# Kernel optimization log

Measured on AMD Instinct MI355X. Metric: run time of the kernel, lower is better.

Reference implementation:

```python
import jax, jax.numpy as jnp
import numpy as np

HEADS = 8
DIM_HEAD = 64
SCALE = DIM_HEAD ** -0.5


def setup_inputs() -> dict:
    key = jax.random.key(0)
    ks = jax.random.split(key, 6)
    b, n, d_model = 16, 1024, 512
    inner = HEADS * DIM_HEAD  # 512
    std = d_model ** -0.5
    return {
        "x": jax.random.normal(ks[0], (b, n, d_model), jnp.float32),
        "Wq": jax.random.normal(ks[1], (inner, d_model), jnp.float32) * std,
        "Wk": jax.random.normal(ks[2], (inner, d_model), jnp.float32) * std,
        "Wv": jax.random.normal(ks[3], (inner, d_model), jnp.float32) * std,
        "rel_bias": jax.random.normal(ks[4], (HEADS, n, n), jnp.float32) * 0.02,
        "Wo": jax.random.normal(ks[5], (d_model, inner), jnp.float32) * std,
        "bo": jnp.zeros((d_model,), jnp.float32),
    }


def reference(x, Wq, Wk, Wv, rel_bias, Wo, bo):
    b, n, _ = x.shape
    # projections (Linear with weight of shape [out, in], no bias)
    def proj_heads(W):
        t = jnp.einsum('bnc,ec->bne', x, W)             # [b, n, inner]
        return t.reshape(b, n, HEADS, DIM_HEAD).transpose(0, 2, 1, 3)  # [b, h, n, d]
    q = proj_heads(Wq)
    k = proj_heads(Wk)
    v = proj_heads(Wv)
    sim = jnp.einsum('bhid,bhjd->bhij', q, k) * SCALE
    sim = sim + rel_bias[None]                          # additive rel-pos bias
    attn = jax.nn.softmax(sim, axis=-1)
    out = jnp.einsum('bhij,bhjd->bhid', attn, v)        # [b, h, n, d]
    out = out.transpose(0, 2, 1, 3).reshape(b, n, HEADS * DIM_HEAD)
    return jnp.einsum('bne,ce->bnc', out, Wo) + bo
```

## Files before the change

kernel.cpp:

```cpp
#include <hip/hip_runtime.h>

typedef unsigned short u16;
typedef short short8 __attribute__((ext_vector_type(8)));
typedef float fx4 __attribute__((ext_vector_type(4)));
typedef u16 u16x4 __attribute__((ext_vector_type(4)));
typedef u16 u16x8 __attribute__((ext_vector_type(8)));


__device__ __forceinline__ u16 f2bf(float f) {
  union { float f; unsigned u; } v; v.f = f;
  unsigned r = (v.u + 0x7fffu + ((v.u >> 16) & 1u)) >> 16;
  return (u16)r;
}
__device__ __forceinline__ float bf2f(u16 u) {
  union { unsigned u; float f; } v; v.u = ((unsigned)u) << 16;
  return v.f;
}
__device__ __forceinline__ void load_lds16(const void* g, void* l) {
  __builtin_amdgcn_global_load_lds((const __attribute__((address_space(1))) void*)g,
                                   (__attribute__((address_space(3))) void*)l, 16, 0, 0);
}
__device__ __forceinline__ int swz(int row, int colb) {
  return (row << 7) | (colb ^ ((row & 7) << 4));
}

__global__ __launch_bounds__(256) void k_convert(
    const float* __restrict__ x, const float* __restrict__ wq, const float* __restrict__ wk,
    const float* __restrict__ wv, const float* __restrict__ wo, const float* __restrict__ bias,
    u16* __restrict__ xb, u16* __restrict__ wqkv, u16* __restrict__ wob, u16* __restrict__ biasb) {
  const int total = 2228224;
  for (int u = blockIdx.x * blockDim.x + threadIdx.x; u < total; u += gridDim.x * blockDim.x) {
    const float* src; u16* dst; int off;
    if (u < 1048576)      { src = x;    dst = xb;            off = u << 3; }
    else if (u < 1081344) { src = wq;   dst = wqkv;          off = (u - 1048576) << 3; }
    else if (u < 1114112) { src = wk;   dst = wqkv + 262144; off = (u - 1081344) << 3; }
    else if (u < 1146880) { src = wv;   dst = wqkv + 524288; off = (u - 1114112) << 3; }
    else if (u < 1179648) { src = wo;   dst = wob;           off = (u - 1146880) << 3; }
    else                  { src = bias; dst = biasb;         off = (u - 1179648) << 3; }
    float4 a = *(const float4*)(src + off);
    float4 b = *(const float4*)(src + off + 4);
    u16x8 o;
    o[0] = f2bf(a.x); o[1] = f2bf(a.y); o[2] = f2bf(a.z); o[3] = f2bf(a.w);
    o[4] = f2bf(b.x); o[5] = f2bf(b.y); o[6] = f2bf(b.z); o[7] = f2bf(b.w);
    *(u16x8*)(dst + off) = o;
  }
}

__device__ __forceinline__ void gemm_core(const u16* __restrict__ A, const u16* __restrict__ Bm,
                                          int mt, int nt, int tid, fx4 acc[4][4],
                                          u16* ldsA, u16* ldsB) {
  const int w = tid >> 6, l = tid & 63;
  const int wr = w >> 1, wc = w & 1;
  const int lr = l & 15, kg = (l >> 4) * 8;
  for (int k0 = 0; k0 < 512; k0 += 32) {
#pragma unroll
    for (int i = 0; i < 2; ++i) {
      int seg = w * 2 + i;
      int idx = seg * 512 + l * 8;
      int row = idx >> 5, col = idx & 31;
      load_lds16(A  + (mt * 128 + row) * 512 + k0 + col, (char*)ldsA + seg * 1024);
      load_lds16(Bm + (nt * 128 + row) * 512 + k0 + col, (char*)ldsB + seg * 1024);
    }
    __syncthreads();
    short8 a[4], b[4];
#pragma unroll
    for (int mi = 0; mi < 4; ++mi) a[mi] = *(const short8*)&ldsA[(wr * 64 + mi * 16 + lr) * 32 + kg];
#pragma unroll
    for (int ni = 0; ni < 4; ++ni) b[ni] = *(const short8*)&ldsB[(wc * 64 + ni * 16 + lr) * 32 + kg];
#pragma unroll
    for (int mi = 0; mi < 4; ++mi)
#pragma unroll
      for (int ni = 0; ni < 4; ++ni)
        acc[mi][ni] = __builtin_amdgcn_mfma_f32_16x16x32_bf16(a[mi], b[ni], acc[mi][ni], 0, 0, 0);
    __syncthreads();
  }
}

__global__ __launch_bounds__(256) void k_proj(const u16* __restrict__ xb, const u16* __restrict__ wqkv,
                                              u16* __restrict__ Qb, u16* __restrict__ Kb,
                                              u16* __restrict__ Vtb) {
  __shared__ u16 ldsA[128 * 32], ldsB[128 * 32];
  int orig = blockIdx.x;
  int wgid = (orig & 7) * 192 + (orig >> 3);
  int mt = wgid / 12, nt = wgid % 12;
  int tid = threadIdx.x;
  fx4 acc[4][4] = {};
  gemm_core(xb, wqkv, mt, nt, tid, acc, ldsA, ldsB);
  const int w = tid >> 6, l = tid & 63, wr = w >> 1, wc = w & 1;
  const int rb = mt * 128 + wr * 64 + ((l >> 4) << 2);
  const int eb = ((nt & 3) << 7) + wc * 64 + (l & 15);
  if (nt < 8) {
    u16* dst = (nt < 4) ? Qb : Kb;
#pragma unroll
    for (int ni = 0; ni < 4; ++ni) {
      int e = eb + ni * 16, hh = e >> 6, d = e & 63;
#pragma unroll
      for (int mi = 0; mi < 4; ++mi)
#pragma unroll
        for (int j = 0; j < 4; ++j) {
          int r = rb + mi * 16 + j, bb = r >> 10, nn = r & 1023;
          dst[(((bb << 3) + hh) * 1024 + nn) * 64 + d] = f2bf(acc[mi][ni][j]);
        }
    }
  } else {
#pragma unroll
    for (int ni = 0; ni < 4; ++ni) {
      int e = eb + ni * 16, hh = e >> 6, d = e & 63;
#pragma unroll
      for (int mi = 0; mi < 4; ++mi) {
        int r0 = rb + mi * 16, bb = r0 >> 10, nn = r0 & 1023;
        u16x4 p;
#pragma unroll
        for (int j = 0; j < 4; ++j) p[j] = f2bf(acc[mi][ni][j]);
        *(u16x4*)&Vtb[(((bb << 3) + hh) * 64 + d) * 1024 + nn] = p;
      }
    }
  }
}

__global__ __launch_bounds__(256) void k_attn(const u16* __restrict__ Qb, const u16* __restrict__ Kb,
                                              const u16* __restrict__ Vtb, const u16* __restrict__ biasb,
                                              u16* __restrict__ Ob) {
  __shared__ u16 ldsK[2][64 * 64], ldsV[2][64 * 64];
  __shared__ u16 ldsP[4][16 * 64];
  int orig = blockIdx.x;
  int wgid = (orig & 7) * 256 + (orig >> 3);
  int h = wgid >> 8, bb = (wgid >> 4) & 15, qt = wgid & 15;
  const int tid = threadIdx.x, w = tid >> 6, l = tid & 63;
  const int lr = l & 15, g = l >> 4;
  const int q0 = qt * 64;
  const u16*  Qbh = Qb + (size_t)((bb * 8 + h) * 1024) * 64;
  const char* Kc  = (const char*)(Kb  + (size_t)((bb * 8 + h) * 1024) * 64);
  const char* Vc  = (const char*)(Vtb + (size_t)((bb * 8 + h) * 64) * 1024);
  const u16* Bt = biasb + ((size_t)h << 20) + (size_t)(q0 + w * 16 + g * 4) * 1024 + lr;
  const int qrow = q0 + w * 16 + lr;
  short8 qf0 = *(const short8*)&Qbh[qrow * 64 + g * 8];
  short8 qf1 = *(const short8*)&Qbh[qrow * 64 + 32 + g * 8];
  float m_r[4], l_r[4];
  fx4 acc_o[4] = {};
#pragma unroll
  for (int j = 0; j < 4; ++j) { m_r[j] = -1e30f; l_r[j] = 0.f; }

  const int segb0 = (w * 2) * 1024, segb1 = (w * 2 + 1) * 1024;
  int o0 = segb0 + l * 16, o1 = segb1 + l * 16;
  int bs0 = o0 ^ (((o0 >> 7) & 7) << 4), bs1 = o1 ^ (((o1 >> 7) & 7) << 4);
  int row0 = bs0 >> 7, colb0 = bs0 & 127;
  int row1 = bs1 >> 7, colb1 = bs1 & 127;

#define STAGE(kt, p)                                                                 \
  {                                                                                  \
    load_lds16(Kc + (size_t)((kt) * 64 + row0) * 128 + colb0, (char*)ldsK[p] + segb0); \
    load_lds16(Vc + (size_t)row0 * 2048 + (kt) * 128 + colb0, (char*)ldsV[p] + segb0); \
    load_lds16(Kc + (size_t)((kt) * 64 + row1) * 128 + colb1, (char*)ldsK[p] + segb1); \
    load_lds16(Vc + (size_t)row1 * 2048 + (kt) * 128 + colb1, (char*)ldsV[p] + segb1); \
  }

  STAGE(0, 0);

  for (int kt = 0; kt < 16; ++kt) {
    const int p = kt & 1;
    u16 br[16];
#pragma unroll
    for (int ct = 0; ct < 4; ++ct)
#pragma unroll
      for (int j = 0; j < 4; ++j)
        br[ct * 4 + j] = Bt[(size_t)j * 1024 + kt * 64 + ct * 16];
    __builtin_amdgcn_sched_barrier(0);
    if (kt < 15) {
      STAGE(kt + 1, p ^ 1);
      __builtin_amdgcn_sched_barrier(0);
      asm volatile("s_waitcnt vmcnt(4)" ::: "memory");
    } else {
      asm volatile("s_waitcnt vmcnt(0)" ::: "memory");
    }
    __builtin_amdgcn_sched_barrier(0);
    __builtin_amdgcn_s_barrier();

    fx4 s[4];
#pragma unroll
    for (int ct = 0; ct < 4; ++ct) {
      short8 kf0 = *(const short8*)((char*)ldsK[p] + swz(ct * 16 + lr, g * 16));
      short8 kf1 = *(const short8*)((char*)ldsK[p] + swz(ct * 16 + lr, 64 + g * 16));
      fx4 t = {};
      t = __builtin_amdgcn_mfma_f32_16x16x32_bf16(qf0, kf0, t, 0, 0, 0);
      t = __builtin_amdgcn_mfma_f32_16x16x32_bf16(qf1, kf1, t, 0, 0, 0);
      s[ct] = t;
    }
#pragma unroll
    for (int ct = 0; ct < 4; ++ct)
#pragma unroll
      for (int j = 0; j < 4; ++j)
        s[ct][j] = s[ct][j] * 0.125f + bf2f(br[ct * 4 + j]);
#pragma unroll
    for (int j = 0; j < 4; ++j) {
      float tm = fmaxf(fmaxf(s[0][j], s[1][j]), fmaxf(s[2][j], s[3][j]));
#pragma unroll
      for (int d = 1; d < 16; d <<= 1) tm = fmaxf(tm, __shfl_xor(tm, d));
      float mn = fmaxf(m_r[j], tm);
      float corr = __expf(m_r[j] - mn);
      m_r[j] = mn;
      float rs = 0.f;
#pragma unroll
      for (int ct = 0; ct < 4; ++ct) { float p2 = __expf(s[ct][j] - mn); s[ct][j] = p2; rs += p2; }
#pragma unroll
      for (int d = 1; d < 16; d <<= 1) rs += __shfl_xor(rs, d);
      l_r[j] = l_r[j] * corr + rs;
#pragma unroll
      for (int dt = 0; dt < 4; ++dt) acc_o[dt][j] *= corr;
    }
    char* Pw = (char*)ldsP[w];
#pragma unroll
    for (int ct = 0; ct < 4; ++ct)
#pragma unroll
      for (int j = 0; j < 4; ++j)
        *(u16*)(Pw + swz(g * 4 + j, (ct * 16 + lr) * 2)) = f2bf(s[ct][j]);
    short8 pf0 = *(const short8*)(Pw + swz(lr, g * 16));
    short8 pf1 = *(const short8*)(Pw + swz(lr, 64 + g * 16));
#pragma unroll
    for (int dt = 0; dt < 4; ++dt) {
      short8 vf0 = *(const short8*)((char*)ldsV[p] + swz(dt * 16 + lr, g * 16));
      short8 vf1 = *(const short8*)((char*)ldsV[p] + swz(dt * 16 + lr, 64 + g * 16));
      acc_o[dt] = __builtin_amdgcn_mfma_f32_16x16x32_bf16(pf0, vf0, acc_o[dt], 0, 0, 0);
      acc_o[dt] = __builtin_amdgcn_mfma_f32_16x16x32_bf16(pf1, vf1, acc_o[dt], 0, 0, 0);
    }
    __builtin_amdgcn_s_barrier();
  }
#undef STAGE
#pragma unroll
  for (int j = 0; j < 4; ++j) {
    float inv = 1.f / l_r[j];
    int q = q0 + w * 16 + g * 4 + j;
#pragma unroll
    for (int dt = 0; dt < 4; ++dt) {
      int col = h * 64 + dt * 16 + lr;
      Ob[(size_t)(bb * 1024 + q) * 512 + col] = f2bf(acc_o[dt][j] * inv);
    }
  }
}

__global__ __launch_bounds__(256) void k_out(const u16* __restrict__ Ob, const u16* __restrict__ Wob,
                                             const float* __restrict__ bo, float* __restrict__ out) {
  __shared__ u16 ldsA[128 * 32], ldsB[128 * 32];
  int orig = blockIdx.x;
  int wgid = (orig & 7) * 64 + (orig >> 3);
  int mt = wgid >> 2, nt = wgid & 3;
  int tid = threadIdx.x;
  fx4 acc[4][4] = {};
  gemm_core(Ob, Wob, mt, nt, tid, acc, ldsA, ldsB);
  const int w = tid >> 6, l = tid & 63, wr = w >> 1, wc = w & 1;
  const int rb = mt * 128 + wr * 64 + ((l >> 4) << 2);
  const int eb = nt * 128 + wc * 64 + (l & 15);
#pragma unroll
  for (int ni = 0; ni < 4; ++ni) {
    int e = eb + ni * 16;
    float bv = bo[e];
#pragma unroll
    for (int mi = 0; mi < 4; ++mi)
#pragma unroll
      for (int j = 0; j < 4; ++j) {
        int r = rb + mi * 16 + j;
        out[(size_t)r * 512 + e] = acc[mi][ni][j] + bv;
      }
  }
}

extern "C" void kernel_launch(void* const* d_in, const int* in_sizes, int n_in,
                              void* d_out, int out_size, void* d_ws, size_t ws_size,
                              hipStream_t stream) {
  const float* x    = (const float*)d_in[0];
  const float* wq   = (const float*)d_in[1];
  const float* wk   = (const float*)d_in[2];
  const float* wv   = (const float*)d_in[3];
  const float* bias = (const float*)d_in[4];
  const float* wo   = (const float*)d_in[5];
  const float* bo   = (const float*)d_in[6];
  float* out = (float*)d_out;
  char* ws = (char*)d_ws;
  u16* xb    = (u16*)(ws + 0);
  u16* wqkv  = (u16*)(ws + 16777216);
  u16* wob   = (u16*)(ws + 18350080);
  u16* biasb = (u16*)(ws + 18874368);
  u16* Qb    = (u16*)(ws + 35651584);
  u16* Kb    = (u16*)(ws + 52428800);
  u16* Vtb   = (u16*)(ws + 69206016);
  u16* Ob    = (u16*)(ws + 85983232);

  hipLaunchKernelGGL(k_convert, dim3(2048), dim3(256), 0, stream,
                     x, wq, wk, wv, wo, bias, xb, wqkv, wob, biasb);
  hipLaunchKernelGGL(k_proj, dim3(1536), dim3(256), 0, stream, xb, wqkv, Qb, Kb, Vtb);
  hipLaunchKernelGGL(k_attn, dim3(2048), dim3(256), 0, stream, Qb, Kb, Vtb, biasb, Ob);
  hipLaunchKernelGGL(k_out, dim3(512), dim3(256), 0, stream, Ob, wob, bo, out);
}
```

Baseline: 282.7 us.

## Double-buffer GEMM LDS loads and switch attention softmax to exp2 domain

The shared GEMM core used by the projection and output kernels now double-buffers its LDS tiles. It prefetches the next K-slice with global_load_lds before computing on the current one, using explicit vmcnt waits and s_barrier in place of two __syncthreads per iteration. Separately, the relative-position bias is pre-multiplied by log2(e) during conversion and the QK scale is folded with log2(e), so the softmax can use exp2f instead of __expf. This doubles LDS use in the GEMM kernels, which may affect occupancy, and slightly changes the rounding of the bf16 bias.

After: 288.3 us. 2.0% more time.

```diff
diff --git a/kernel.cpp b/kernel.cpp
--- a/kernel.cpp
+++ b/kernel.cpp
@@ -30,18 +30,18 @@
     u16* __restrict__ xb, u16* __restrict__ wqkv, u16* __restrict__ wob, u16* __restrict__ biasb) {
   const int total = 2228224;
   for (int u = blockIdx.x * blockDim.x + threadIdx.x; u < total; u += gridDim.x * blockDim.x) {
-    const float* src; u16* dst; int off;
+    const float* src; u16* dst; int off; float fac = 1.0f;
     if (u < 1048576)      { src = x;    dst = xb;            off = u << 3; }
     else if (u < 1081344) { src = wq;   dst = wqkv;          off = (u - 1048576) << 3; }
     else if (u < 1114112) { src = wk;   dst = wqkv + 262144; off = (u - 1081344) << 3; }
     else if (u < 1146880) { src = wv;   dst = wqkv + 524288; off = (u - 1114112) << 3; }
     else if (u < 1179648) { src = wo;   dst = wob;           off = (u - 1146880) << 3; }
-    else                  { src = bias; dst = biasb;         off = (u - 1179648) << 3; }
+    else { src = bias; dst = biasb; off = (u - 1179648) << 3; fac = 1.44269504089f; }
     float4 a = *(const float4*)(src + off);
     float4 b = *(const float4*)(src + off + 4);
     u16x8 o;
-    o[0] = f2bf(a.x); o[1] = f2bf(a.y); o[2] = f2bf(a.z); o[3] = f2bf(a.w);
-    o[4] = f2bf(b.x); o[5] = f2bf(b.y); o[6] = f2bf(b.z); o[7] = f2bf(b.w);
+    o[0] = f2bf(a.x * fac); o[1] = f2bf(a.y * fac); o[2] = f2bf(a.z * fac); o[3] = f2bf(a.w * fac);
+    o[4] = f2bf(b.x * fac); o[5] = f2bf(b.y * fac); o[6] = f2bf(b.z * fac); o[7] = f2bf(b.w * fac);
     *(u16x8*)(dst + off) = o;
   }
 }
@@ -52,34 +52,57 @@
   const int w = tid >> 6, l = tid & 63;
   const int wr = w >> 1, wc = w & 1;
   const int lr = l & 15, kg = (l >> 4) * 8;
-  for (int k0 = 0; k0 < 512; k0 += 32) {
-#pragma unroll
-    for (int i = 0; i < 2; ++i) {
-      int seg = w * 2 + i;
-      int idx = seg * 512 + l * 8;
-      int row = idx >> 5, col = idx & 31;
-      load_lds16(A  + (mt * 128 + row) * 512 + k0 + col, (char*)ldsA + seg * 1024);
-      load_lds16(Bm + (nt * 128 + row) * 512 + k0 + col, (char*)ldsB + seg * 1024);
-    }
-    __syncthreads();
+  const int seg0 = w * 2, seg1 = w * 2 + 1;
+  const int idx0 = seg0 * 512 + l * 8, idx1 = seg1 * 512 + l * 8;
+  const int row0 = idx0 >> 5, col0 = idx0 & 31;
+  const int row1 = idx1 >> 5, col1 = idx1 & 31;
+  const u16* Ab = A  + (size_t)(mt * 128) * 512;
+  const u16* Bb = Bm + (size_t)(nt * 128) * 512;
+
+#define GSTAGE(k0, p)                                                              \
+  {                                                                                \
+    load_lds16(Ab + row0 * 512 + (k0) + col0, (char*)ldsA + (p) * 8192 + seg0 * 1024); \
+    load_lds16(Bb + row0 * 512 + (k0) + col0, (char*)ldsB + (p) * 8192 + seg0 * 1024); \
+    load_lds16(Ab + row1 * 512 + (k0) + col1, (char*)ldsA + (p) * 8192 + seg1 * 1024); \
+    load_lds16(Bb + row1 * 512 + (k0) + col1, (char*)ldsB + (p) * 8192 + seg1 * 1024); \
+  }
+
+  GSTAGE(0, 0);
+
+  for (int kt = 0; kt < 16; ++kt) {
+    const int p = kt & 1;
+    __builtin_amdgcn_sched_barrier(0);
+    if (kt < 15) {
+      GSTAGE((kt + 1) * 32, p ^ 1);
+      __builtin_amdgcn_sched_barrier(0);
+      asm volatile("s_waitcnt vmcnt(4)" ::: "memory");
+    } else {
+      asm volatile("s_waitcnt vmcnt(0)" ::: "memory");
+    }
+    __builtin_amdgcn_sched_barrier(0);
+    __builtin_amdgcn_s_barrier();
+
     short8 a[4], b[4];
 #pragma unroll
-    for (int mi = 0; mi < 4; ++mi) a[mi] = *(const short8*)&ldsA[(wr * 64 + mi * 16 + lr) * 32 + kg];
-#pragma unroll
-    for (int ni = 0; ni < 4; ++ni) b[ni] = *(const short8*)&ldsB[(wc * 64 + ni * 16 + lr) * 32 + kg];
+    for (int mi = 0; mi < 4; ++mi)
+      a[mi] = *(const short8*)&ldsA[p * 4096 + (wr * 64 + mi * 16 + lr) * 32 + kg];
+#pragma unroll
+    for (int ni = 0; ni < 4; ++ni)
+      b[ni] = *(const short8*)&ldsB[p * 4096 + (wc * 64 + ni * 16 + lr) * 32 + kg];
 #pragma unroll
     for (int mi = 0; mi < 4; ++mi)
 #pragma unroll
       for (int ni = 0; ni < 4; ++ni)
         acc[mi][ni] = __builtin_amdgcn_mfma_f32_16x16x32_bf16(a[mi], b[ni], acc[mi][ni], 0, 0, 0);
-    __syncthreads();
-  }
+    __builtin_amdgcn_s_barrier();
+  }
+#undef GSTAGE
 }
 
 __global__ __launch_bounds__(256) void k_proj(const u16* __restrict__ xb, const u16* __restrict__ wqkv,
                                               u16* __restrict__ Qb, u16* __restrict__ Kb,
                                               u16* __restrict__ Vtb) {
-  __shared__ u16 ldsA[128 * 32], ldsB[128 * 32];
+  __shared__ u16 ldsA[2 * 128 * 32], ldsB[2 * 128 * 32];
   int orig = blockIdx.x;
   int wgid = (orig & 7) * 192 + (orig >> 3);
   int mt = wgid / 12, nt = wgid % 12;
@@ -136,6 +159,7 @@
   const int qrow = q0 + w * 16 + lr;
   short8 qf0 = *(const short8*)&Qbh[qrow * 64 + g * 8];
   short8 qf1 = *(const short8*)&Qbh[qrow * 64 + 32 + g * 8];
+  const float SC2 = 0.125f * 1.44269504089f;
   float m_r[4], l_r[4];
   fx4 acc_o[4] = {};
 #pragma unroll
@@ -190,18 +214,18 @@
     for (int ct = 0; ct < 4; ++ct)
 #pragma unroll
       for (int j = 0; j < 4; ++j)
-        s[ct][j] = s[ct][j] * 0.125f + bf2f(br[ct * 4 + j]);
+        s[ct][j] = s[ct][j] * SC2 + bf2f(br[ct * 4 + j]);
 #pragma unroll
     for (int j = 0; j < 4; ++j) {
       float tm = fmaxf(fmaxf(s[0][j], s[1][j]), fmaxf(s[2][j], s[3][j]));
 #pragma unroll
       for (int d = 1; d < 16; d <<= 1) tm = fmaxf(tm, __shfl_xor(tm, d));
       float mn = fmaxf(m_r[j], tm);
-      float corr = __expf(m_r[j] - mn);
+      float corr = exp2f(m_r[j] - mn);
       m_r[j] = mn;
       float rs = 0.f;
 #pragma unroll
-      for (int ct = 0; ct < 4; ++ct) { float p2 = __expf(s[ct][j] - mn); s[ct][j] = p2; rs += p2; }
+      for (int ct = 0; ct < 4; ++ct) { float p2 = exp2f(s[ct][j] - mn); s[ct][j] = p2; rs += p2; }
 #pragma unroll
       for (int d = 1; d < 16; d <<= 1) rs += __shfl_xor(rs, d);
       l_r[j] = l_r[j] * corr + rs;
@@ -240,7 +264,7 @@
 
 __global__ __launch_bounds__(256) void k_out(const u16* __restrict__ Ob, const u16* __restrict__ Wob,
                                              const float* __restrict__ bo, float* __restrict__ out) {
-  __shared__ u16 ldsA[128 * 32], ldsB[128 * 32];
+  __shared__ u16 ldsA[2 * 128 * 32], ldsB[2 * 128 * 32];
   int orig = blockIdx.x;
   int wgid = (orig & 7) * 64 + (orig >> 3);
   int mt = wgid >> 2, nt = wgid & 3;
```
